# Performance work log

Hardware: AMD Instinct MI355X
Metric: run time of the kernel (lower is better)

Reference implementation:

```python
import jax, jax.numpy as jnp
import numpy as np

N_NODES = 50000


def _inv_sqrt_deg(idx, n):
    # degree per node from an edge-endpoint index vector; 0-degree -> norm 0 (DGL behavior)
    deg = jax.ops.segment_sum(jnp.ones(idx.shape[0], jnp.float32), idx, num_segments=n)
    return jnp.where(deg > 0, jax.lax.rsqrt(jnp.maximum(deg, 1.0)), 0.0)


def _graph_conv(x, src, dst, W, b, norm_src, norm_dst, n):
    # DGL GraphConv, norm='both': D_dst^{-1/2} A D_src^{-1/2} X W + b
    h = (x * norm_src[:, None]) @ W            # [N, out]
    agg = jax.ops.segment_sum(h[src], dst, num_segments=n)  # SpMM via gather+scatter-add
    return agg * norm_dst[:, None] + b


def setup_inputs() -> dict:
    key = jax.random.key(0)
    ks = jax.random.split(key, 8)
    N, E, D, H, C = N_NODES, 800000, 64, 64, 10
    s = 1.0 / np.sqrt(H)
    return {
        "x": jax.random.normal(ks[0], (N, D), jnp.float32),
        "src": jax.random.randint(ks[1], (E,), 0, N, jnp.int32),
        "dst": jax.random.randint(ks[2], (E,), 0, N, jnp.int32),
        "W1": jax.random.normal(ks[3], (D, H), jnp.float32) * s,
        "b1": jnp.zeros((H,), jnp.float32),
        "W2": jax.random.normal(ks[4], (H, H), jnp.float32) * s,
        "b2": jnp.zeros((H,), jnp.float32),
        "W3": jax.random.normal(ks[5], (H, H), jnp.float32) * s,
        "b3": jnp.zeros((H,), jnp.float32),
        "Wfc": jax.random.normal(ks[6], (H, C), jnp.float32) * s,
        "bfc": jnp.zeros((C,), jnp.float32),
    }


def reference(x, src, dst, W1, b1, W2, b2, W3, b3, Wfc, bfc):
    n = x.shape[0]
    norm_src = _inv_sqrt_deg(src, n)  # out-degree^{-1/2}
    norm_dst = _inv_sqrt_deg(dst, n)  # in-degree^{-1/2}
    h = jnp.tanh(_graph_conv(x, src, dst, W1, b1, norm_src, norm_dst, n))
    h = jnp.tanh(_graph_conv(h, src, dst, W2, b2, norm_src, norm_dst, n))
    h = jnp.tanh(_graph_conv(h, src, dst, W3, b3, norm_src, norm_dst, n))
    return h @ Wfc + bfc
```

## Files before the change

### kernel.cpp

```cpp
#include <hip/hip_runtime.h>
#include <hip/hip_fp16.h>
#include <math.h>

#define THREADS 256
#define CHUNK_SHIFT 14
#define CHUNK (1 << CHUNK_SHIFT)
#define LDS_WORDS 12500

__global__ __launch_bounds__(1024)
void k_hist(const int* __restrict__ src, const int* __restrict__ dst,
            unsigned int* __restrict__ partS, unsigned int* __restrict__ partD,
            unsigned char* __restrict__ rank, int E, int P, int words) {
    __shared__ unsigned int hist[LDS_WORDS];
    int isSrc = (blockIdx.x >= (unsigned)P);
    int b = isSrc ? (blockIdx.x - P) : blockIdx.x;
    int tid = threadIdx.x;

    for (int w = tid; w < words; w += 1024) hist[w] = 0u;
    __syncthreads();

    int start = b << CHUNK_SHIFT;
    int end = start + CHUNK; if (end > E) end = E;

    if (isSrc) {
        for (int e = start + tid; e < end; e += 1024) {
            int s = src[e];
            atomicAdd(&hist[s >> 2], 1u << ((s & 3) * 8));
        }
    } else {
        for (int e = start + tid; e < end; e += 1024) {
            int d = dst[e];
            unsigned int old = atomicAdd(&hist[d >> 2], 1u << ((d & 3) * 8));
            rank[e] = (unsigned char)((old >> ((d & 3) * 8)) & 0xFFu);
        }
    }
    __syncthreads();

    unsigned int* part = isSrc ? partS : partD;
    for (int w = tid; w < words; w += 1024)
        part[(size_t)b * words + w] = hist[w];
}

__global__ __launch_bounds__(THREADS)
void k_pre(const unsigned int* __restrict__ partS,
           const unsigned int* __restrict__ partD,
           unsigned int* __restrict__ prefD,
           int* __restrict__ deg_d, float* __restrict__ ns, float* __restrict__ nd,
           int* __restrict__ rp, int* __restrict__ bsum,
           int P, int words, int N) {
    __shared__ int sdeg[THREADS];
    int t = threadIdx.x;
    int i = blockIdx.x * THREADS + t;

    int c = 0, s = 0;
    if (i < N) {
        int w = i >> 2;
        int sh = (i & 3) * 8;
        unsigned char* pB = (unsigned char*)prefD;
        for (int b = 0; b < P; b++) {
            size_t off = (size_t)b * words + w;
            unsigned int v = (partD[off] >> sh) & 0xFFu;
            pB[off * 4 + (i & 3)] = (unsigned char)c;
            c += (int)v;
        }
        for (int b = 0; b < P; b++)
            s += (int)((partS[(size_t)b * words + w] >> sh) & 0xFFu);
        deg_d[i] = c;
        nd[i] = c ? 1.0f / sqrtf((float)c) : 0.0f;
        ns[i] = s ? 1.0f / sqrtf((float)s) : 0.0f;
    }
    sdeg[t] = (i < N) ? c : 0;
    __syncthreads();

    int run = sdeg[t];
    for (int off = 1; off < THREADS; off <<= 1) {
        int x = (t >= off) ? sdeg[t - off] : 0;
        __syncthreads();
        sdeg[t] += x;
        __syncthreads();
    }
    if (i < N) rp[i] = sdeg[t] - run;
    if (t == THREADS - 1) bsum[blockIdx.x] = sdeg[t];
}

__global__ void k_scan2(int* __restrict__ bsum, int nb) {
    __shared__ int s[THREADS];
    int t = threadIdx.x;
    int v = (t < nb) ? bsum[t] : 0;
    s[t] = v;
    __syncthreads();
    for (int off = 1; off < THREADS; off <<= 1) {
        int x = (t >= off) ? s[t - off] : 0;
        __syncthreads();
        s[t] += x;
        __syncthreads();
    }
    if (t < nb) bsum[t] = s[t] - v;
}

__global__ void k_fill(const int* __restrict__ src, const int* __restrict__ dst,
                       const int* __restrict__ rp, const int* __restrict__ bsum,
                       const unsigned char* __restrict__ rank,
                       const unsigned int* __restrict__ prefD,
                       int* __restrict__ col, int E, int words) {
    int e = blockIdx.x * blockDim.x + threadIdx.x;
    if (e < E) {
        int d = dst[e];
        int b = e >> CHUNK_SHIFT;
        unsigned int pk = prefD[(size_t)b * words + (d >> 2)];
        int pref = (int)((pk >> ((d & 3) * 8)) & 0xFFu);
        col[rp[d] + bsum[d >> 8] + pref + (int)rank[e]] = src[e];
    }
}

#define XS_STRIDE 68
__global__ __launch_bounds__(256, 4)
void k_gemm64(const float* __restrict__ X, const float* __restrict__ norm,
              const float* __restrict__ W, __half* __restrict__ H, int N) {
    __shared__ float Xs[64 * XS_STRIDE];
    __shared__ float Ws[64 * 64];
    int tid = threadIdx.x;
    int rowBase = blockIdx.x * 64;

    for (int i = tid; i < 1024; i += 256)
        ((float4*)Ws)[i] = ((const float4*)W)[i];
    for (int i = tid; i < 1024; i += 256) {
        int r  = i >> 4;
        int k4 = i & 15;
        int row = rowBase + r;
        float4 v = make_float4(0.f, 0.f, 0.f, 0.f);
        if (row < N) {
            v = ((const float4*)X)[(size_t)row * 16 + k4];
            float nv = norm[row];
            v.x *= nv; v.y *= nv; v.z *= nv; v.w *= nv;
        }
        *((float4*)&Xs[r * XS_STRIDE + (k4 << 2)]) = v;
    }
    __syncthreads();

    int tc = tid & 15;
    int tr = tid >> 4;
    int c0 = tc * 4, r0 = tr * 4;
    float acc[4][4] = {};

#pragma unroll 2
    for (int k = 0; k < 64; k += 4) {
        float4 wv[4];
#pragma unroll
        for (int kk = 0; kk < 4; kk++)
            wv[kk] = *((const float4*)&Ws[(k + kk) * 64 + c0]);
#pragma unroll
        for (int j = 0; j < 4; j++) {
            float4 xv = *((const float4*)&Xs[(r0 + j) * XS_STRIDE + k]);
            acc[j][0] += xv.x * wv[0].x; acc[j][1] += xv.x * wv[0].y;
            acc[j][2] += xv.x * wv[0].z; acc[j][3] += xv.x * wv[0].w;
            acc[j][0] += xv.y * wv[1].x; acc[j][1] += xv.y * wv[1].y;
            acc[j][2] += xv.y * wv[1].z; acc[j][3] += xv.y * wv[1].w;
            acc[j][0] += xv.z * wv[2].x; acc[j][1] += xv.z * wv[2].y;
            acc[j][2] += xv.z * wv[2].z; acc[j][3] += xv.z * wv[2].w;
            acc[j][0] += xv.w * wv[3].x; acc[j][1] += xv.w * wv[3].y;
            acc[j][2] += xv.w * wv[3].z; acc[j][3] += xv.w * wv[3].w;
        }
    }
#pragma unroll
    for (int j = 0; j < 4; j++) {
        int row = rowBase + r0 + j;
        if (row < N) {
            __half2 h01 = __floats2half2_rn(acc[j][0], acc[j][1]);
            __half2 h23 = __floats2half2_rn(acc[j][2], acc[j][3]);
            uint2 pk;
            pk.x = *(unsigned int*)&h01;
            pk.y = *(unsigned int*)&h23;
            *((uint2*)(H + (size_t)row * 64 + c0)) = pk;
        }
    }
}

__global__ __launch_bounds__(256)
void k_agg(const uint4* __restrict__ H4, const int* __restrict__ rp,
           const int* __restrict__ bsum, const int* __restrict__ deg,
           const int* __restrict__ col, const float* __restrict__ nd,
           const float* __restrict__ bias, float* __restrict__ Out, int N) {
    int wave = threadIdx.x >> 6;
    int lane = threadIdx.x & 63;
    int stride = gridDim.x * 4;
    int node = blockIdx.x * 4 + wave;
    if (node >= N) return;
    int g = lane >> 3;
    int l = lane & 7;

    int g0 = (lane >> 3) & 1, g1 = (lane >> 4) & 1, g2 = (lane >> 5) & 1;
    int ch = (l << 3) + (g0 << 2) + (g1 << 1) + g2;
    float bv = bias[ch];

    int start = rp[node] + bsum[node >> 8];
    int n = deg[node];
    float nv = nd[node];

    while (true) {
        int nextNode = node + stride;
        int nStart = 0, nN = 0;
        float nNv = 0.0f;
        if (nextNode < N) {
            nStart = rp[nextNode] + bsum[nextNode >> 8];
            nN = deg[nextNode];
            nNv = nd[nextNode];
        }

        int sStart = __builtin_amdgcn_readfirstlane(start);
        int sN     = __builtin_amdgcn_readfirstlane(n);
        float a[8] = {0.f, 0.f, 0.f, 0.f, 0.f, 0.f, 0.f, 0.f};

        auto accum = [&](uint4 v) {
            float2 f0 = __half22float2(*(__half2*)&v.x);
            float2 f1 = __half22float2(*(__half2*)&v.y);
            float2 f2 = __half22float2(*(__half2*)&v.z);
            float2 f3 = __half22float2(*(__half2*)&v.w);
            a[0] += f0.x; a[1] += f0.y; a[2] += f1.x; a[3] += f1.y;
            a[4] += f2.x; a[5] += f2.y; a[6] += f3.x; a[7] += f3.y;
        };

        if (sN <= 32) {
            int idx = (lane < sN) ? col[sStart + lane] : 0;
            int s0 = __shfl(idx, g);
            uint4 z; z.x = 0u; z.y = 0u; z.z = 0u; z.w = 0u;
            uint4 v0 = z, v1 = z, v2 = z, v3 = z;
            if (g < sN) v0 = H4[(size_t)s0 * 8 + l];
            if (sN > 8) {
                int s1 = __shfl(idx, 8 + g);
                if (8 + g < sN) v1 = H4[(size_t)s1 * 8 + l];
            }
            if (sN > 16) {
                int s2 = __shfl(idx, 16 + g);
                if (16 + g < sN) v2 = H4[(size_t)s2 * 8 + l];
            }
            if (sN > 24) {
                int s3 = __shfl(idx, 24 + g);
                if (24 + g < sN) v3 = H4[(size_t)s3 * 8 + l];
            }
            accum(v0);
            if (sN > 8)  accum(v1);
            if (sN > 16) accum(v2);
            if (sN > 24) accum(v3);
        } else {
            for (int base = 0; base < sN; base += 64) {
                int cnt = sN - base;
                if (cnt > 64) cnt = 64;
                int idx = (lane < cnt) ? col[sStart + base + lane] : 0;
                int j = 0;
                for (; j + 32 <= cnt; j += 32) {
                    int s0 = __shfl(idx, j + g);
                    int s1 = __shfl(idx, j + 8 + g);
                    int s2 = __shfl(idx, j + 16 + g);
                    int s3 = __shfl(idx, j + 24 + g);
                    uint4 v0 = H4[(size_t)s0 * 8 + l];
                    uint4 v1 = H4[(size_t)s1 * 8 + l];
                    uint4 v2 = H4[(size_t)s2 * 8 + l];
                    uint4 v3 = H4[(size_t)s3 * 8 + l];
                    accum(v0); accum(v1); accum(v2); accum(v3);
                }
                for (; j + 8 <= cnt; j += 8) {
                    int s0 = __shfl(idx, j + g);
                    uint4 v0 = H4[(size_t)s0 * 8 + l];
                    accum(v0);
                }
                int t = cnt - j;
                if (t > 0) {
                    int s0 = __shfl(idx, j + (g < t ? g : 0));
                    if (g < t) {
                        uint4 v0 = H4[(size_t)s0 * 8 + l];
                        accum(v0);
                    }
                }
            }
        }

        float b_[4];
#pragma unroll
        for (int j = 0; j < 4; j++) {
            float send = g0 ? a[j] : a[j + 4];
            float recv = __shfl_xor(send, 8);
            float keep = g0 ? a[j + 4] : a[j];
            b_[j] = keep + recv;
        }
        float c_[2];
#pragma unroll
        for (int j = 0; j < 2; j++) {
            float send = g1 ? b_[j] : b_[j + 2];
            float recv = __shfl_xor(send, 16);
            float keep = g1 ? b_[j + 2] : b_[j];
            c_[j] = keep + recv;
        }
        float send = g2 ? c_[0] : c_[1];
        float recv = __shfl_xor(send, 32);
        float keep = g2 ? c_[1] : c_[0];
        float s = keep + recv;

        Out[(size_t)node * 64 + ch] = tanhf(s * nv + bv);

        if (nextNode >= N) break;
        node = nextNode; start = nStart; n = nN; nv = nNv;
    }
}

__global__ __launch_bounds__(640)
void k_fc(const float* __restrict__ X, const float* __restrict__ W,
          const float* __restrict__ b, float* __restrict__ out, int N) {
    __shared__ float Ws[640];
    __shared__ float bs[10];
    __shared__ float Xs[64 * 65];
    int tid = threadIdx.x;
    Ws[tid] = W[tid];
    if (tid < 10) bs[tid] = b[tid];
    int nodeBase = blockIdx.x * 64;
    for (int i = tid; i < 4096; i += 640) {
        int r = i >> 6, cc = i & 63;
        int nn = nodeBase + r;
        Xs[r * 65 + cc] = (nn < N) ? X[(size_t)nn * 64 + cc] : 0.0f;
    }
    __syncthreads();
    int ln = tid / 10, cl = tid % 10;
    float acc = bs[cl];
#pragma unroll
    for (int k = 0; k < 64; k++)
        acc += Xs[ln * 65 + k] * Ws[k * 10 + cl];
    int node = nodeBase + ln;
    if (node < N) out[(size_t)node * 10 + cl] = acc;
}

extern "C" void kernel_launch(void* const* d_in, const int* in_sizes, int n_in,
                              void* d_out, int out_size, void* d_ws, size_t ws_size,
                              hipStream_t stream) {
    const float* x   = (const float*)d_in[0];
    const int*   src = (const int*)d_in[1];
    const int*   dst = (const int*)d_in[2];
    const float* W1  = (const float*)d_in[3];
    const float* b1  = (const float*)d_in[4];
    const float* W2  = (const float*)d_in[5];
    const float* b2  = (const float*)d_in[6];
    const float* W3  = (const float*)d_in[7];
    const float* b3  = (const float*)d_in[8];
    const float* Wfc = (const float*)d_in[9];
    const float* bfc = (const float*)d_in[10];
    float* out = (float*)d_out;
    int N = in_sizes[0] / 64;
    int E = in_sizes[1];
    int P = (E + CHUNK - 1) >> CHUNK_SHIFT;
    int words = (N + 3) / 4;

    char* ws = (char*)d_ws;
    size_t p = 0;
    auto alloc = [&](size_t bytes) -> void* {
        void* r = ws + p;
        p = (p + bytes + 255) & ~(size_t)255;
        return r;
    };
    int*    deg_d = (int*)alloc((size_t)N * 4);
    int*    rp    = (int*)alloc((size_t)N * 4);
    int*    bsum  = (int*)alloc((size_t)THREADS * 4);
    unsigned char* rank = (unsigned char*)alloc((size_t)E);
    int*    col   = (int*)alloc((size_t)E * 4);
    float*  ns    = (float*)alloc((size_t)N * 4);
    float*  nd    = (float*)alloc((size_t)N * 4);
    unsigned int* partS = (unsigned int*)alloc((size_t)P * words * 4);
    unsigned int* partD = (unsigned int*)alloc((size_t)P * words * 4);
    unsigned int* prefD = (unsigned int*)alloc((size_t)P * words * 4);
    __half* bufH  = (__half*)alloc((size_t)N * 64 * 2);
    float*  bufX  = (float*)alloc((size_t)N * 64 * 4);
    (void)ws_size; (void)n_in; (void)out_size;

    int gE = (E + THREADS - 1) / THREADS;
    int gN = (N + THREADS - 1) / THREADS;

    k_hist <<<2 * P, 1024, 0, stream>>>(src, dst, partS, partD, rank, E, P, words);
    k_pre  <<<gN, THREADS, 0, stream>>>(partS, partD, prefD, deg_d, ns, nd,
                                        rp, bsum, P, words, N);
    k_scan2<<<1,  THREADS, 0, stream>>>(bsum, gN);
    k_fill <<<gE, THREADS, 0, stream>>>(src, dst, rp, bsum, rank, prefD, col, E, words);

    int gG = (N + 63) / 64;
    int gA = 2048;
    int gF = (N + 63) / 64;

    k_gemm64<<<gG, 256, 0, stream>>>(x,    ns, W1, bufH, N);
    k_agg   <<<gA, 256, 0, stream>>>((const uint4*)bufH, rp, bsum, deg_d, col, nd,
                                     b1, bufX, N);
    k_gemm64<<<gG, 256, 0, stream>>>(bufX, ns, W2, bufH, N);
    k_agg   <<<gA, 256, 0, stream>>>((const uint4*)bufH, rp, bsum, deg_d, col, nd,
                                     b2, bufX, N);
    k_gemm64<<<gG, 256, 0, stream>>>(bufX, ns, W3, bufH, N);
    k_agg   <<<gA, 256, 0, stream>>>((const uint4*)bufH, rp, bsum, deg_d, col, nd,
                                     b3, bufX, N);
    k_fc    <<<gF, 640, 0, stream>>>(bufX, Wfc, bfc, out, N);
}
```

Measured before the change: 229.7 us.

## Fuse aggregation with next-layer GEMM and FC, merge CSR fill with first GEMM

Each aggregation kernel now processes a 64-node tile. It writes the tanh outputs, already scaled by the source norm, into shared memory, then runs the next layer's 64x64 GEMM, or the final 64x10 FC, in the same kernel. This removes the fp32 intermediate buffer round trip and three launches. The CSR fill and the first GEMM share one launch with disjoint block ranges. The prefix kernel is rewritten: each 256-thread block splits the partition loop four ways per histogram word. A global atomic counter hands out block offsets, which replaces the separate scan kernel. In exchange, each wave handles 16 nodes serially and the aggregation grid is smaller than the earlier grid-stride launch.

```diff
diff --git a/kernel.cpp b/kernel.cpp
--- a/kernel.cpp
+++ b/kernel.cpp
@@ -6,12 +6,16 @@
 #define CHUNK_SHIFT 14
 #define CHUNK (1 << CHUNK_SHIFT)
 #define LDS_WORDS 12500
+#define MAXB 16
+#define XS_STRIDE 68
 
 __global__ __launch_bounds__(1024)
 void k_hist(const int* __restrict__ src, const int* __restrict__ dst,
             unsigned int* __restrict__ partS, unsigned int* __restrict__ partD,
-            unsigned char* __restrict__ rank, int E, int P, int words) {
+            unsigned char* __restrict__ rank, unsigned int* __restrict__ counter,
+            int E, int P, int words) {
     __shared__ unsigned int hist[LDS_WORDS];
+    if (blockIdx.x == 0 && threadIdx.x == 0) *counter = 0u;
     int isSrc = (blockIdx.x >= (unsigned)P);
     int b = isSrc ? (blockIdx.x - P) : blockIdx.x;
     int tid = threadIdx.x;
@@ -47,81 +51,119 @@
            unsigned int* __restrict__ prefD,
            int* __restrict__ deg_d, float* __restrict__ ns, float* __restrict__ nd,
            int* __restrict__ rp, int* __restrict__ bsum,
+           unsigned int* __restrict__ counter,
            int P, int words, int N) {
-    __shared__ int sdeg[THREADS];
+    __shared__ unsigned int qsD[4][64];
+    __shared__ unsigned int qsS[4][64];
     int t = threadIdx.x;
-    int i = blockIdx.x * THREADS + t;
-
-    int c = 0, s = 0;
-    if (i < N) {
-        int w = i >> 2;
-        int sh = (i & 3) * 8;
-        unsigned char* pB = (unsigned char*)prefD;
-        for (int b = 0; b < P; b++) {
-            size_t off = (size_t)b * words + w;
-            unsigned int v = (partD[off] >> sh) & 0xFFu;
-            pB[off * 4 + (i & 3)] = (unsigned char)c;
-            c += (int)v;
-        }
-        for (int b = 0; b < P; b++)
-            s += (int)((partS[(size_t)b * words + w] >> sh) & 0xFFu);
-        deg_d[i] = c;
-        nd[i] = c ? 1.0f / sqrtf((float)c) : 0.0f;
-        ns[i] = s ? 1.0f / sqrtf((float)s) : 0.0f;
-    }
-    sdeg[t] = (i < N) ? c : 0;
+    int widx = t & 63;
+    int q = t >> 6;
+    int w = blockIdx.x * 64 + widx;
+    bool valid = (w < words);
+
+    int per = (P + 3) >> 2;
+    int blo = q * per;
+    int cnt = P - blo; if (cnt > per) cnt = per; if (cnt < 0) cnt = 0;
+
+    unsigned int vD[MAXB];
+    unsigned int runD = 0, runS = 0;
+#pragma unroll
+    for (int bb = 0; bb < MAXB; bb++) {
+        unsigned int vd = 0, vs = 0;
+        if (bb < cnt && valid) {
+            size_t off = (size_t)(blo + bb) * words + w;
+            vd = partD[off];
+            vs = partS[off];
+        }
+        vD[bb] = vd;
+        runD += vd;
+        runS += vs;
+    }
+    qsD[q][widx] = runD;
+    qsS[q][widx] = runS;
     __syncthreads();
 
-    int run = sdeg[t];
-    for (int off = 1; off < THREADS; off <<= 1) {
-        int x = (t >= off) ? sdeg[t - off] : 0;
-        __syncthreads();
-        sdeg[t] += x;
-        __syncthreads();
-    }
-    if (i < N) rp[i] = sdeg[t] - run;
-    if (t == THREADS - 1) bsum[blockIdx.x] = sdeg[t];
+    unsigned int baseD = 0, totD = 0, totS = 0;
+#pragma unroll
+    for (int qq = 0; qq < 4; qq++) {
+        unsigned int xd = qsD[qq][widx];
+        unsigned int xs = qsS[qq][widx];
+        if (qq < q) baseD += xd;
+        totD += xd;
+        totS += xs;
+    }
+
+    unsigned int pref = baseD;
+#pragma unroll
+    for (int bb = 0; bb < MAXB; bb++) {
+        if (bb < cnt && valid)
+            prefD[(size_t)(blo + bb) * words + w] = pref;
+        pref += vD[bb];
+    }
+
+    if (q == 0) {
+        int b0 = (int)(totD & 0xFFu), b1 = (int)((totD >> 8) & 0xFFu),
+            b2 = (int)((totD >> 16) & 0xFFu), b3 = (int)((totD >> 24) & 0xFFu);
+        int wsum = b0 + b1 + b2 + b3;
+        int incl = wsum;
+#pragma unroll
+        for (int off = 1; off < 64; off <<= 1) {
+            int y = __shfl_up(incl, off);
+            if (widx >= off) incl += y;
+        }
+        int excl = incl - wsum;
+        int btot = __shfl(incl, 63);
+        if (widx == 0)
+            bsum[blockIdx.x] = (int)atomicAdd(counter, (unsigned int)btot);
+        if (valid) {
+            int s0 = (int)(totS & 0xFFu), s1 = (int)((totS >> 8) & 0xFFu),
+                s2 = (int)((totS >> 16) & 0xFFu), s3 = (int)((totS >> 24) & 0xFFu);
+            int4 dv; dv.x = b0; dv.y = b1; dv.z = b2; dv.w = b3;
+            *(int4*)&deg_d[(size_t)4 * w] = dv;
+            float4 ndv;
+            ndv.x = b0 ? 1.0f / sqrtf((float)b0) : 0.0f;
+            ndv.y = b1 ? 1.0f / sqrtf((float)b1) : 0.0f;
+            ndv.z = b2 ? 1.0f / sqrtf((float)b2) : 0.0f;
+            ndv.w = b3 ? 1.0f / sqrtf((float)b3) : 0.0f;
+            *(float4*)&nd[(size_t)4 * w] = ndv;
+            float4 nsv;
+            nsv.x = s0 ? 1.0f / sqrtf((float)s0) : 0.0f;
+            nsv.y = s1 ? 1.0f / sqrtf((float)s1) : 0.0f;
+            nsv.z = s2 ? 1.0f / sqrtf((float)s2) : 0.0f;
+            nsv.w = s3 ? 1.0f / sqrtf((float)s3) : 0.0f;
+            *(float4*)&ns[(size_t)4 * w] = nsv;
+            int4 rv; rv.x = excl; rv.y = excl + b0;
+            rv.z = excl + b0 + b1; rv.w = excl + b0 + b1 + b2;
+            *(int4*)&rp[(size_t)4 * w] = rv;
+        }
+    }
 }
 
-__global__ void k_scan2(int* __restrict__ bsum, int nb) {
-    __shared__ int s[THREADS];
-    int t = threadIdx.x;
-    int v = (t < nb) ? bsum[t] : 0;
-    s[t] = v;
-    __syncthreads();
-    for (int off = 1; off < THREADS; off <<= 1) {
-        int x = (t >= off) ? s[t - off] : 0;
-        __syncthreads();
-        s[t] += x;
-        __syncthreads();
-    }
-    if (t < nb) bsum[t] = s[t] - v;
-}
-
-__global__ void k_fill(const int* __restrict__ src, const int* __restrict__ dst,
-                       const int* __restrict__ rp, const int* __restrict__ bsum,
-                       const unsigned char* __restrict__ rank,
-                       const unsigned int* __restrict__ prefD,
-                       int* __restrict__ col, int E, int words) {
-    int e = blockIdx.x * blockDim.x + threadIdx.x;
-    if (e < E) {
-        int d = dst[e];
-        int b = e >> CHUNK_SHIFT;
-        unsigned int pk = prefD[(size_t)b * words + (d >> 2)];
-        int pref = (int)((pk >> ((d & 3) * 8)) & 0xFFu);
-        col[rp[d] + bsum[d >> 8] + pref + (int)rank[e]] = src[e];
-    }
-}
-
-#define XS_STRIDE 68
 __global__ __launch_bounds__(256, 4)
-void k_gemm64(const float* __restrict__ X, const float* __restrict__ norm,
-              const float* __restrict__ W, __half* __restrict__ H, int N) {
+void k_fill_gemm(const int* __restrict__ src, const int* __restrict__ dst,
+                 const int* __restrict__ rp, const int* __restrict__ bsum,
+                 const unsigned char* __restrict__ rank,
+                 const unsigned int* __restrict__ prefD,
+                 int* __restrict__ col, int E, int words, int gFill,
+                 const float* __restrict__ X, const float* __restrict__ norm,
+                 const float* __restrict__ W, __half* __restrict__ H, int N) {
     __shared__ float Xs[64 * XS_STRIDE];
     __shared__ float Ws[64 * 64];
     int tid = threadIdx.x;
-    int rowBase = blockIdx.x * 64;
-
+
+    if ((int)blockIdx.x < gFill) {
+        int e = blockIdx.x * 256 + tid;
+        if (e < E) {
+            int d = dst[e];
+            int b = e >> CHUNK_SHIFT;
+            unsigned int pk = prefD[(size_t)b * words + (d >> 2)];
+            int pref = (int)((pk >> ((d & 3) * 8)) & 0xFFu);
+            col[rp[d] + bsum[d >> 8] + pref + (int)rank[e]] = src[e];
+        }
+        return;
+    }
+
+    int rowBase = ((int)blockIdx.x - gFill) * 64;
     for (int i = tid; i < 1024; i += 256)
         ((float4*)Ws)[i] = ((const float4*)W)[i];
     for (int i = tid; i < 1024; i += 256) {
@@ -176,35 +218,59 @@
     }
 }
 
-__global__ __launch_bounds__(256)
-void k_agg(const uint4* __restrict__ H4, const int* __restrict__ rp,
-           const int* __restrict__ bsum, const int* __restrict__ deg,
-           const int* __restrict__ col, const float* __restrict__ nd,
-           const float* __restrict__ bias, float* __restrict__ Out, int N) {
-    int wave = threadIdx.x >> 6;
-    int lane = threadIdx.x & 63;
-    int stride = gridDim.x * 4;
-    int node = blockIdx.x * 4 + wave;
-    if (node >= N) return;
+template<int FC>
+__global__ __launch_bounds__(256, 4)
+void k_agg_gemm(const uint4* __restrict__ H4, const int* __restrict__ rp,
+                const int* __restrict__ bsum, const int* __restrict__ deg,
+                const int* __restrict__ col, const float* __restrict__ nd,
+                const float* __restrict__ nsrc, const float* __restrict__ bias,
+                const float* __restrict__ W, const float* __restrict__ Wb2,
+                void* __restrict__ OutP, int N) {
+    __shared__ float Xs[64 * XS_STRIDE];
+    __shared__ float Ws[FC ? 640 : 4096];
+    __shared__ float Wb[16];
+    int tid = threadIdx.x;
+
+    if constexpr (FC == 0) {
+        for (int i = tid; i < 1024; i += 256)
+            ((float4*)Ws)[i] = ((const float4*)W)[i];
+    } else {
+        for (int i = tid; i < 640; i += 256) {
+            int k = i / 10, c = i - k * 10;
+            Ws[c * 64 + k] = W[i];
+        }
+        if (tid < 10) Wb[tid] = Wb2[tid];
+    }
+
+    int wave = tid >> 6;
+    int lane = tid & 63;
     int g = lane >> 3;
     int l = lane & 7;
-
     int g0 = (lane >> 3) & 1, g1 = (lane >> 4) & 1, g2 = (lane >> 5) & 1;
     int ch = (l << 3) + (g0 << 2) + (g1 << 1) + g2;
     float bv = bias[ch];
-
-    int start = rp[node] + bsum[node >> 8];
-    int n = deg[node];
-    float nv = nd[node];
-
-    while (true) {
-        int nextNode = node + stride;
+    int rowBase = blockIdx.x * 64;
+
+    int node = rowBase + wave * 16;
+    int start = 0, n = 0;
+    float nv = 0.f, nsv = 0.f;
+    if (node < N) {
+        start = rp[node] + bsum[node >> 8];
+        n = deg[node];
+        nv = nd[node];
+        if constexpr (FC == 0) nsv = nsrc[node];
+    }
+
+#pragma unroll 1
+    for (int i = 0; i < 16; i++) {
+        int nextNode = node + 1;
         int nStart = 0, nN = 0;
-        float nNv = 0.0f;
-        if (nextNode < N) {
+        float nNv = 0.f, nNs = 0.f;
+        if (i < 15 && nextNode < N) {
             nStart = rp[nextNode] + bsum[nextNode >> 8];
             nN = deg[nextNode];
             nNv = nd[nextNode];
+            if constexpr (FC == 0) nNs = nsrc[nextNode];
         }
 
         int sStart = __builtin_amdgcn_readfirstlane(start);
@@ -264,10 +330,10 @@
                     uint4 v0 = H4[(size_t)s0 * 8 + l];
                     accum(v0);
                 }
-                int t = cnt - j;
-                if (t > 0) {
-                    int s0 = __shfl(idx, j + (g < t ? g : 0));
-                    if (g < t) {
+                int tl = cnt - j;
+                if (tl > 0) {
+                    int s0 = __shfl(idx, j + (g < tl ? g : 0));
+                    if (g < tl) {
                         uint4 v0 = H4[(size_t)s0 * 8 + l];
                         accum(v0);
                     }
@@ -296,36 +362,73 @@
         float keep = g2 ? c_[1] : c_[0];
         float s = keep + recv;
 
-        Out[(size_t)node * 64 + ch] = tanhf(s * nv + bv);
-
-        if (nextNode >= N) break;
-        node = nextNode; start = nStart; n = nN; nv = nNv;
-    }
-}
-
-__global__ __launch_bounds__(640)
-void k_fc(const float* __restrict__ X, const float* __restrict__ W,
-          const float* __restrict__ b, float* __restrict__ out, int N) {
-    __shared__ float Ws[640];
-    __shared__ float bs[10];
-    __shared__ float Xs[64 * 65];
-    int tid = threadIdx.x;
-    Ws[tid] = W[tid];
-    if (tid < 10) bs[tid] = b[tid];
-    int nodeBase = blockIdx.x * 64;
-    for (int i = tid; i < 4096; i += 640) {
-        int r = i >> 6, cc = i & 63;
-        int nn = nodeBase + r;
-        Xs[r * 65 + cc] = (nn < N) ? X[(size_t)nn * 64 + cc] : 0.0f;
+        float tv = tanhf(s * nv + bv);
+        float val;
+        if constexpr (FC == 0) val = tv * nsv;
+        else                   val = tv;
+        Xs[(wave * 16 + i) * XS_STRIDE + ch] = (node < N) ? val : 0.0f;
+
+        node = nextNode; start = nStart; n = nN; nv = nNv; nsv = nNs;
     }
     __syncthreads();
-    int ln = tid / 10, cl = tid % 10;
-    float acc = bs[cl];
-#pragma unroll
-    for (int k = 0; k < 64; k++)
-        acc += Xs[ln * 65 + k] * Ws[k * 10 + cl];
-    int node = nodeBase + ln;
-    if (node < N) out[(size_t)node * 10 + cl] = acc;
+
+    if constexpr (FC == 0) {
+        __half* Hh = (__half*)OutP;
+        int tc = tid & 15;
+        int tr = tid >> 4;
+        int c0 = tc * 4, r0 = tr * 4;
+        float acc[4][4] = {};
+
+#pragma unroll 2
+        for (int k = 0; k < 64; k += 4) {
+            float4 wv[4];
+#pragma unroll
+            for (int kk = 0; kk < 4; kk++)
+                wv[kk] = *((const float4*)&Ws[(k + kk) * 64 + c0]);
+#pragma unroll
+            for (int j = 0; j < 4; j++) {
+                float4 xv = *((const float4*)&Xs[(r0 + j) * XS_STRIDE + k]);
+                acc[j][0] += xv.x * wv[0].x; acc[j][1] += xv.x * wv[0].y;
+                acc[j][2] += xv.x * wv[0].z; acc[j][3] += xv.x * wv[0].w;
+                acc[j][0] += xv.y * wv[1].x; acc[j][1] += xv.y * wv[1].y;
+                acc[j][2] += xv.y * wv[1].z; acc[j][3] += xv.y * wv[1].w;
+                acc[j][0] += xv.z * wv[2].x; acc[j][1] += xv.z * wv[2].y;
+                acc[j][2] += xv.z * wv[2].z; acc[j][3] += xv.z * wv[2].w;
+                acc[j][0] += xv.w * wv[3].x; acc[j][1] += xv.w * wv[3].y;
+                acc[j][2] += xv.w * wv[3].z; acc[j][3] += xv.w * wv[3].w;
+            }
+        }
+#pragma unroll
+        for (int j = 0; j < 4; j++) {
+            int row = rowBase + r0 + j;
+            if (row < N) {
+                __half2 h01 = __floats2half2_rn(acc[j][0], acc[j][1]);
+                __half2 h23 = __floats2half2_rn(acc[j][2], acc[j][3]);
+                uint2 pk;
+                pk.x = *(unsigned int*)&h01;
+                pk.y = *(unsigned int*)&h23;
+                *((uint2*)(Hh + (size_t)row * 64 + c0)) = pk;
+            }
+        }
+    } else {
+        float* outF = (float*)OutP;
+        for (int idx = tid; idx < 640; idx += 256) {
+            int ln = idx / 10;
+            int cl = idx - ln * 10;
+            float acc = Wb[cl];
+#pragma unroll
+            for (int k = 0; k < 64; k += 4) {
+                float4 xv = *((const float4*)&Xs[ln * XS_STRIDE + k]);
+                float4 wv = *((const float4*)&Ws[cl * 64 + k]);
+                acc += xv.x * wv.x;
+                acc += xv.y * wv.y;
+                acc += xv.z * wv.z;
+                acc += xv.w * wv.w;
+            }
+            int row = rowBase + ln;
+            if (row < N) outF[(size_t)row * 10 + cl] = acc;
+        }
+    }
 }
 
 extern "C" void kernel_launch(void* const* d_in, const int* in_sizes, int n_in,
@@ -366,30 +469,24 @@
     unsigned int* partD = (unsigned int*)alloc((size_t)P * words * 4);
     unsigned int* prefD = (unsigned int*)alloc((size_t)P * words * 4);
     __half* bufH  = (__half*)alloc((size_t)N * 64 * 2);
-    float*  bufX  = (float*)alloc((size_t)N * 64 * 4);
+    __half* bufH2 = (__half*)alloc((size_t)N * 64 * 2);
+    unsigned int* counter = (unsigned int*)alloc(4);
     (void)ws_size; (void)n_in; (void)out_size;
 
-    int gE = (E + THREADS - 1) / THREADS;
-    int gN = (N + THREADS - 1) / THREADS;
-
-    k_hist <<<2 * P, 1024, 0, stream>>>(src, dst, partS, partD, rank, E, P, words);
-    k_pre  <<<gN, THREADS, 0, stream>>>(partS, partD, prefD, deg_d, ns, nd,
-                                        rp, bsum, P, words, N);
-    k_scan2<<<1,  THREADS, 0, stream>>>(bsum, gN);
-    k_fill <<<gE, THREADS, 0, stream>>>(src, dst, rp, bsum, rank, prefD, col, E, words);
-
+    int gFill = (E + 255) / 256;
+    int gP = (words + 63) / 64;
     int gG = (N + 63) / 64;
-    int gA = 2048;
-    int gF = (N + 63) / 64;
-
-    k_gemm64<<<gG, 256, 0, stream>>>(x,    ns, W1, bufH, N);
-    k_agg   <<<gA, 256, 0, stream>>>((const uint4*)bufH, rp, bsum, deg_d, col, nd,
-                                     b1, bufX, N);
-    k_gemm64<<<gG, 256, 0, stream>>>(bufX, ns, W2, bufH, N);
-    k_agg   <<<gA, 256, 0, stream>>>((const uint4*)bufH, rp, bsum, deg_d, col, nd,
-                                     b2, bufX, N);
-    k_gemm64<<<gG, 256, 0, stream>>>(bufX, ns, W3, bufH, N);
-    k_agg   <<<gA, 256, 0, stream>>>((const uint4*)bufH, rp, bsum, deg_d, col, nd,
-                                     b3, bufX, N);
-    k_fc    <<<gF, 640, 0, stream>>>(bufX, Wfc, bfc, out, N);
+
+    k_hist<<<2 * P, 1024, 0, stream>>>(src, dst, partS, partD, rank, counter, E, P, words);
+    k_pre <<<gP, THREADS, 0, stream>>>(partS, partD, prefD, deg_d, ns, nd,
+                                       rp, bsum, counter, P, words, N);
+    k_fill_gemm<<<gFill + gG, 256, 0, stream>>>(src, dst, rp, bsum, rank, prefD,
+                                                col, E, words, gFill,
+                                                x, ns, W1, bufH, N);
+    k_agg_gemm<0><<<gG, 256, 0, stream>>>((const uint4*)bufH,  rp, bsum, deg_d, col,
+                                          nd, ns, b1, W2, nullptr, bufH2, N);
+    k_agg_gemm<0><<<gG, 256, 0, stream>>>((const uint4*)bufH2, rp, bsum, deg_d, col,
+                                          nd, ns, b2, W3, nullptr, bufH, N);
+    k_agg_gemm<1><<<gG, 256, 0, stream>>>((const uint4*)bufH,  rp, bsum, deg_d, col,
+                                          nd, ns, b3, Wfc, bfc, out, N);
 }
```

After: 215.3 us. -6.2%, faster.
